# Optimization experiments

Measured on AMD Instinct MI355X. Metric: run time of the kernel, lower is better.

The kernel has to match this reference:

```python
import jax, jax.numpy as jnp
import numpy as np
from jax import lax

BITWIDTH = 7
EPS = 1e-5


def ti_quant(x):
    """TiFloatToInt8: per-tensor int8 quantization with power-of-2 scale."""
    rng = jnp.max(jnp.abs(x))
    bw = jnp.ceil(jnp.log2(rng))
    exp = bw - BITWIDTH
    q = jnp.clip(jnp.round(x * 2.0 ** (BITWIDTH - bw)), -128.0, 127.0)
    return q, exp


def ti_conv(xv, xe, wv, we, pad):
    """TiConv2d: integer conv (simulated in f32, all values int-valued),
    int32 accumulate, then shift back to 8 bits; exponents add."""
    acc = lax.conv_general_dilated(
        xv, wv, window_strides=(1, 1), padding=[(pad, pad), (pad, pad)],
        dimension_numbers=("NCHW", "OIHW", "NCHW"))
    rng = jnp.max(jnp.abs(acc))
    bw = jnp.ceil(jnp.log2(rng))
    shift = jnp.maximum(bw - BITWIDTH, 0.0)
    q = jnp.clip(jnp.round(acc * 2.0 ** (-shift)), -128.0, 127.0)
    return q, xe + we + shift


def batchnorm(x, gamma, beta):
    # training-mode BN: batch statistics over (N, H, W)
    mean = jnp.mean(x, axis=(0, 2, 3), keepdims=True)
    var = jnp.var(x, axis=(0, 2, 3), keepdims=True)
    g = gamma[None, :, None, None]
    b = beta[None, :, None, None]
    return g * (x - mean) * lax.rsqrt(var + EPS) + b


def setup_inputs() -> dict:
    key = jax.random.key(0)
    k0, k1, k2, k3, k4 = jax.random.split(key, 5)
    B, Cin, Cout, H, W = 32, 128, 256, 56, 56
    x_val = jax.random.randint(k0, (B, Cin, H, W), -128, 128, dtype=jnp.int32)
    x_exp = jnp.zeros((), jnp.float32) - 7.0
    wDW = jnp.round(jnp.clip(jax.random.normal(k1, (Cin, Cin, 3, 3), jnp.float32) * 32.0, -128.0, 127.0))
    wDW_exp = jnp.zeros((), jnp.float32) - 9.0
    wPW = jnp.round(jnp.clip(jax.random.normal(k2, (Cout, Cin, 1, 1), jnp.float32) * 32.0, -128.0, 127.0))
    wPW_exp = jnp.zeros((), jnp.float32) - 9.0
    gamma1 = jnp.ones((Cin,), jnp.float32) + 0.1 * jax.random.normal(k3, (Cin,), jnp.float32)
    beta1 = jnp.zeros((Cin,), jnp.float32)
    gamma2 = jnp.ones((Cout,), jnp.float32) + 0.1 * jax.random.normal(k4, (Cout,), jnp.float32)
    beta2 = jnp.zeros((Cout,), jnp.float32)
    return {"x_val": x_val, "x_exp": x_exp, "wDW": wDW, "wDW_exp": wDW_exp,
            "wPW": wPW, "wPW_exp": wPW_exp, "gamma1": gamma1, "beta1": beta1,
            "gamma2": gamma2, "beta2": beta2}


def reference(x_val, x_exp, wDW, wDW_exp, wPW, wPW_exp, gamma1, beta1, gamma2, beta2):
    xv = x_val.astype(jnp.float32)
    # convDW (3x3, in->in, pad=1)
    q, e = ti_conv(xv, x_exp, wDW, wDW_exp, 1)
    # dequant -> bn1 -> quant
    f = batchnorm(q * 2.0 ** e, gamma1, beta1)
    q, e = ti_quant(f)
    # TiReLU on int values
    q = jnp.maximum(q, 0.0)
    # convPW (1x1, in->out)
    q, e = ti_conv(q, e, wPW, wPW_exp, 0)
    # dequant -> bn2 -> quant -> relu
    f = batchnorm(q * 2.0 ** e, gamma2, beta2)
    q, e = ti_quant(f)
    q = jnp.maximum(q, 0.0)
    return q.astype(jnp.int8), e
```

## Files before the change

kernel.cpp:

```cpp
#include <hip/hip_runtime.h>
#include <cstdint>
#include <cstddef>

#define C1 128
#define C2 256
#define Hh 56
#define Wd 56
#define HW 3136
#define NHW 100352
#define N1 ((size_t)12845056)
#define N2 ((size_t)25690112)
#define XPSZ ((size_t)13778944)

typedef int v4i __attribute__((ext_vector_type(4)));
typedef int v16i __attribute__((ext_vector_type(16)));

static constexpr size_t OFF_XP = 0;
static constexpr size_t OFF_ACC1 = XPSZ;
static constexpr size_t OFF_Q1 = OFF_ACC1 + 4 * N1;
static constexpr size_t OFF_Q3 = OFF_Q1 + N1;
static constexpr size_t OFF_WQ1 = OFF_Q3 + N2;
static constexpr size_t OFF_WQ2 = OFF_WQ1 + 147456;
static constexpr size_t OFF_STATS = OFF_WQ2 + 32768;

struct Stats {
  int absmax1, absmax2, tick1, tick2;
  float scale1, e1, s2, e2;
  float scaleq2, e3, sf, ef;
  int sum1[C1]; unsigned sumsq1[C1];
  int min1[C1], max1[C1];
  float A1[C1], B1c[C1];
  int sum2[C2]; unsigned sumsq2[C2];
  int min2[C2], max2[C2];
  float A2[C2], B2c[C2];
};

__global__ __launch_bounds__(256) void k_pre(
    const int* __restrict__ x, signed char* __restrict__ xp,
    const float* __restrict__ wDW, signed char* __restrict__ wq1t,
    const float* __restrict__ wPW, signed char* __restrict__ wq2t,
    Stats* st) {
  __shared__ signed char lds[56 * 132];
  int t = threadIdx.x, bid = blockIdx.x;
  if (bid < 1856) {
    int hh = bid % 58, n = bid / 58;
    int* xpw = (int*)(xp + ((size_t)n * 58 + hh) * 7424);
    if (hh == 0 || hh == 57) {
      for (int o = t; o < 1856; o += 256) xpw[o] = 0;
      return;
    }
    int h = hh - 1;
    const int* xb = x + (size_t)n * C1 * HW + h * 56;
    for (int idx = t; idx < 7168; idx += 256) {
      int c = idx / 56, w = idx - c * 56;
      lds[w * 132 + c] = (signed char)xb[(size_t)c * HW + w];
    }
    __syncthreads();
    for (int o = t; o < 1856; o += 256) {
      int kb = o / 232, r = o - kb * 232, ww = r >> 2, cw = r & 3;
      int val = (ww == 0 || ww == 57) ? 0
                : *(const int*)&lds[(ww - 1) * 132 + kb * 16 + cw * 4];
      xpw[o] = val;
    }
    return;
  }
  if (bid < 2432) {
    int idx = (bid - 1856) * 256 + t;
    int co = idx / 1152, r = idx - co * 1152;
    int ci = r / 9, pos = r - ci * 9;
    int k = pos * 128 + ci;
    wq1t[(size_t)(k >> 4) * 2048 + co * 16 + (k & 15)] = (signed char)(int)wDW[idx];
    return;
  }
  if (bid < 2560) {
    int i = (bid - 2432) * 256 + t;
    int co = i >> 7, ci = i & 127;
    wq2t[(size_t)(ci >> 4) * 4096 + co * 16 + (ci & 15)] = (signed char)(int)wPW[i];
    return;
  }
  if (t == 0) { st->absmax1 = 0; st->absmax2 = 0; st->tick1 = 0; st->tick2 = 0; }
  for (int c = t; c < C1; c += 256) {
    st->sum1[c] = 0; st->sumsq1[c] = 0; st->min1[c] = 127; st->max1[c] = -128;
  }
  for (int c = t; c < C2; c += 256) {
    st->sum2[c] = 0; st->sumsq2[c] = 0; st->min2[c] = 127; st->max2[c] = -128;
  }
}

__device__ inline v4i ld16_lds(const signed char* p) {
  const int2* q = (const int2*)p;
  int2 lo = q[0], hi = q[1];
  v4i r; r[0] = lo.x; r[1] = lo.y; r[2] = hi.x; r[3] = hi.y;
  return r;
}

__device__ inline float bn_affine_v(int sum, unsigned sumsq, int mn, int mx,
                                    float g, float b, float e_in,
                                    float* Aout, float* Bout) {
  double meanq = (double)sum / (double)NHW;
  double varq = (double)sumsq / (double)NHW - meanq * meanq;
  float se = exp2f(e_in);
  float mean = (float)meanq * se;
  float var = (float)varq * se * se;
  float rsq = 1.0f / sqrtf(var + 1e-5f);
  float Avv = g * se * rsq;
  float Bvv = b - g * mean * rsq;
  *Aout = Avv; *Bout = Bvv;
  return fmaxf(fabsf(Avv * (float)mn + Bvv), fabsf(Avv * (float)mx + Bvv));
}

__global__ __launch_bounds__(256, 2) void k_conv1s(
    const signed char* __restrict__ xp, const signed char* __restrict__ wq1t,
    int* __restrict__ acc1, Stats* st) {
  __shared__ int reda[4];
  int t = threadIdx.x, lane = t & 63, wave = t >> 6;
  int half = lane >> 5, l31 = lane & 31;
  size_t g0 = (size_t)blockIdx.x * 256;

  const signed char* ab[2];
#pragma unroll
  for (int i = 0; i < 2; ++i) {
    size_t gm = g0 + wave * 64 + i * 32 + l31;
    int n = (int)(gm / HW);
    int p = (int)(gm - (size_t)n * HW);
    int h = p / 56, w = p - h * 56;
    ab[i] = xp + ((size_t)n * 58 + h) * 7424 + w * 16 + half * 928;
  }
  const signed char* bb[4];
#pragma unroll
  for (int j = 0; j < 4; ++j)
    bb[j] = wq1t + (size_t)(j * 32 + l31) * 16 + half * 2048;

  v16i a1[2][4];
#pragma unroll
  for (int i = 0; i < 2; ++i)
#pragma unroll
    for (int j = 0; j < 4; ++j)
#pragma unroll
      for (int r = 0; r < 16; ++r) a1[i][j][r] = 0;

#pragma unroll
  for (int pos = 0; pos < 9; ++pos) {
    int kh = pos / 3, kw = pos - kh * 3;
    const signed char* a0p = ab[0] + kh * 7424 + kw * 16;
    const signed char* a1p = ab[1] + kh * 7424 + kw * 16;
#pragma unroll
    for (int kb = 0; kb < 8; kb += 2) {
      v4i af0 = *(const v4i*)(a0p + kb * 928);
      v4i af1 = *(const v4i*)(a1p + kb * 928);
      v4i bf[4];
#pragma unroll
      for (int j = 0; j < 4; ++j)
        bf[j] = *(const v4i*)(bb[j] + pos * 16384 + kb * 2048);
#pragma unroll
      for (int j = 0; j < 4; ++j) {
        a1[0][j] = __builtin_amdgcn_mfma_i32_32x32x32_i8(af0, bf[j], a1[0][j], 0, 0, 0);
        a1[1][j] = __builtin_amdgcn_mfma_i32_32x32x32_i8(af1, bf[j], a1[1][j], 0, 0, 0);
      }
    }
  }

  int am = 0;
#pragma unroll
  for (int i = 0; i < 2; ++i)
#pragma unroll
    for (int j = 0; j < 4; ++j)
#pragma unroll
      for (int r = 0; r < 16; ++r) am = max(am, abs(a1[i][j][r]));
  for (int off = 32; off; off >>= 1) am = max(am, __shfl_down(am, off, 64));
  if (lane == 0) reda[wave] = am;
  __syncthreads();
  if (t == 0)
    atomicMax(&st->absmax1, max(max(reda[0], reda[1]), max(reda[2], reda[3])));

  int* ob = acc1 + (size_t)blockIdx.x * 32768;
#pragma unroll
  for (int i = 0; i < 2; ++i)
#pragma unroll
    for (int j = 0; j < 4; ++j)
#pragma unroll
      for (int reg = 0; reg < 16; ++reg)
        ob[(((wave * 2 + i) * 4 + j) * 16 + reg) * 64 + lane] = a1[i][j][reg];
}

__global__ __launch_bounds__(256, 2) void k_qstats1(
    const int* __restrict__ acc1, signed char* __restrict__ q1, Stats* st,
    const float* __restrict__ x_exp, const float* __restrict__ wDW_exp,
    const float* __restrict__ gamma1, const float* __restrict__ beta1) {
  __shared__ int qti[256 * 34];
  __shared__ int psum[C1], psq[C1], pmn[C1], pmx[C1];
  __shared__ float redc[2];
  __shared__ int lastf;
  signed char* qt = (signed char*)qti;
  int t = threadIdx.x, lane = t & 63, wave = t >> 6;
  int half = lane >> 5, l31 = lane & 31;

  if (t < C1) { psum[t] = 0; psq[t] = 0; pmn[t] = 127; pmx[t] = -128; }
  __syncthreads();

  int v1 = st->absmax1;
  int pw = 31 - __clz(v1 | 1);
  int bw = ((v1 & (v1 - 1)) == 0) ? pw : pw + 1;
  int sh = max(bw - 7, 0);
  float scale1 = exp2f((float)(-sh));
  float e1 = x_exp[0] + wDW_exp[0] + (float)sh;
  if (blockIdx.x == 0 && t == 0) st->e1 = e1;

  const int* ib = acc1 + (size_t)blockIdx.x * 32768;
#pragma unroll
  for (int j = 0; j < 4; ++j) {
    int sj = 0, sqj = 0, mnj = 127, mxj = -128;
    int c = j * 32 + l31;
#pragma unroll
    for (int i = 0; i < 2; ++i)
#pragma unroll
      for (int reg = 0; reg < 16; ++reg) {
        int av = ib[(((wave * 2 + i) * 4 + j) * 16 + reg) * 64 + lane];
        int row = (reg & 3) + 8 * (reg >> 2) + 4 * half;
        int pix = wave * 64 + i * 32 + row;
        float r = rintf((float)av * scale1);
        r = fminf(fmaxf(r, -128.f), 127.f);
        int qi = (int)r;
        qt[pix * 136 + c] = (signed char)qi;
        sj += qi; sqj += qi * qi; mnj = min(mnj, qi); mxj = max(mxj, qi);
      }
    sj += __shfl_down(sj, 32, 64);
    sqj += __shfl_down(sqj, 32, 64);
    mnj = min(mnj, __shfl_down(mnj, 32, 64));
    mxj = max(mxj, __shfl_down(mxj, 32, 64));
    if (half == 0) {
      atomicAdd(&psum[c], sj); atomicAdd(&psq[c], sqj);
      atomicMin(&pmn[c], mnj); atomicMax(&pmx[c], mxj);
    }
  }
  __syncthreads();
  if (t < C1) {
    atomicAdd(&st->sum1[t], psum[t]);
    atomicAdd(&st->sumsq1[t], (unsigned)psq[t]);
    atomicMin(&st->min1[t], pmn[t]);
    atomicMax(&st->max1[t], pmx[t]);
  }
  int* q1w = (int*)(q1 + (size_t)blockIdx.x * 256 * 128);
  for (int idx = t; idx < 8192; idx += 256)
    q1w[idx] = qti[(idx >> 5) * 34 + (idx & 31)];

  __syncthreads();
  if (t == 0) lastf = (atomicAdd(&st->tick1, 1) == 391);
  __syncthreads();
  if (lastf) {
    if (t < C1) {
      int sm = atomicAdd(&st->sum1[t], 0);
      unsigned sq = atomicAdd(&st->sumsq1[t], 0u);
      int mn = atomicMin(&st->min1[t], 127);
      int mx = atomicMax(&st->max1[t], -128);
      float cand = bn_affine_v(sm, sq, mn, mx, gamma1[t], beta1[t], e1,
                               &st->A1[t], &st->B1c[t]);
      for (int off = 32; off; off >>= 1) cand = fmaxf(cand, __shfl_down(cand, off, 64));
      if ((t & 63) == 0) redc[t >> 6] = cand;
    }
    __syncthreads();
    if (t == 0) {
      float rng = fmaxf(redc[0], redc[1]);
      float bwv = ceilf(log2f(rng));
      st->s2 = exp2f(7.0f - bwv);
      st->e2 = bwv - 7.0f;
    }
  }
}

template <int STORE>
__global__ __launch_bounds__(256, 2) void k_conv2t(
    const signed char* __restrict__ q1, const signed char* __restrict__ wq2t,
    signed char* __restrict__ q3, Stats* st, const float* __restrict__ wPW_exp,
    const float* __restrict__ gamma2, const float* __restrict__ beta2,
    float* __restrict__ out) {
  __shared__ int qti[128 * 34];
  __shared__ signed char stg[128 * 264];
  __shared__ int psum[C2], psq[C2], pmn[C2], pmx[C2];
  __shared__ int reda[4];
  __shared__ float red2[4];
  __shared__ int lastf;
  signed char* qt = (signed char*)qti;

  int t = threadIdx.x, lane = t & 63, wave = t >> 6;
  int half = lane >> 5, l31 = lane & 31;
  size_t g0 = (size_t)blockIdx.x * 128;

  if (STORE) { psum[t] = 0; psq[t] = 0; pmn[t] = 127; pmx[t] = -128; }

  int c4 = t & 31;
  float Av[4], Bv[4];
#pragma unroll
  for (int jj = 0; jj < 4; ++jj) {
    Av[jj] = st->A1[c4 * 4 + jj];
    Bv[jj] = st->B1c[c4 * 4 + jj];
  }
  float s2 = st->s2;
  const int* q1w = (const int*)(q1 + g0 * 128);
#pragma unroll
  for (int k = 0; k < 16; ++k) {
    int idx = k * 256 + t;
    int v = q1w[idx];
    int pix = idx >> 5;
    int outv = 0;
#pragma unroll
    for (int jj = 0; jj < 4; ++jj) {
      int b = (signed char)(v >> (8 * jj));
      float y = Av[jj] * (float)b + Bv[jj];
      float r = rintf(y * s2);
      r = fminf(fmaxf(r, -128.f), 127.f);
      r = fmaxf(r, 0.f);
      outv |= ((int)r & 0xff) << (8 * jj);
    }
    qti[pix * 34 + c4] = outv;
  }
  __syncthreads();

  v16i acc[8];
#pragma unroll
  for (int j = 0; j < 8; ++j)
#pragma unroll
    for (int r = 0; r < 16; ++r) acc[j][r] = 0;

#pragma unroll
  for (int ks = 0; ks < 4; ++ks) {
    v4i af = ld16_lds(&qt[(wave * 32 + l31) * 136 + half * 16 + ks * 32]);
#pragma unroll
    for (int j = 0; j < 8; ++j) {
      v4i bf = *(const v4i*)(wq2t + (size_t)(ks * 2 + half) * 4096 + (j * 32 + l31) * 16);
      acc[j] = __builtin_amdgcn_mfma_i32_32x32x32_i8(af, bf, acc[j], 0, 0, 0);
    }
  }

  if (STORE == 0) {
    int am2 = 0;
#pragma unroll
    for (int j = 0; j < 8; ++j)
#pragma unroll
      for (int r = 0; r < 16; ++r) am2 = max(am2, abs(acc[j][r]));
    for (int off = 32; off; off >>= 1) am2 = max(am2, __shfl_down(am2, off, 64));
    if (lane == 0) reda[wave] = am2;
    __syncthreads();
    if (t == 0)
      atomicMax(&st->absmax2, max(max(reda[0], reda[1]), max(reda[2], reda[3])));
  } else {
    int v2 = st->absmax2;
    int pw = 31 - __clz(v2 | 1);
    int bw = ((v2 & (v2 - 1)) == 0) ? pw : pw + 1;
    int sh2 = max(bw - 7, 0);
    float scale2 = exp2f((float)(-sh2));
    float e3 = st->e2 + wPW_exp[0] + (float)sh2;
    if (blockIdx.x == 0 && t == 0) st->e3 = e3;
#pragma unroll
    for (int j = 0; j < 8; ++j) {
      int c = j * 32 + l31;
      int sj = 0, sqj = 0, mnj = 127, mxj = -128;
#pragma unroll
      for (int reg = 0; reg < 16; ++reg) {
        int row = (reg & 3) + 8 * (reg >> 2) + 4 * half;
        float r = rintf((float)acc[j][reg] * scale2);
        r = fminf(fmaxf(r, -128.f), 127.f);
        int qi = (int)r;
        stg[(wave * 32 + row) * 264 + c] = (signed char)qi;
        sj += qi; sqj += qi * qi; mnj = min(mnj, qi); mxj = max(mxj, qi);
      }
      sj += __shfl_down(sj, 32, 64);
      sqj += __shfl_down(sqj, 32, 64);
      mnj = min(mnj, __shfl_down(mnj, 32, 64));
      mxj = max(mxj, __shfl_down(mxj, 32, 64));
      if (half == 0) {
        atomicAdd(&psum[c], sj); atomicAdd(&psq[c], sqj);
        atomicMin(&pmn[c], mnj); atomicMax(&pmx[c], mxj);
      }
    }
    __syncthreads();
    atomicAdd(&st->sum2[t], psum[t]);
    atomicAdd(&st->sumsq2[t], (unsigned)psq[t]);
    atomicMin(&st->min2[t], pmn[t]);
    atomicMax(&st->max2[t], pmx[t]);
    int* q3w = (int*)(q3 + g0 * 256);
#pragma unroll
    for (int k = 0; k < 32; ++k) {
      int idx = k * 256 + t;
      int pix = idx >> 6, cw = idx & 63;
      q3w[idx] = *(const int*)&stg[pix * 264 + cw * 4];
    }

    __syncthreads();
    if (t == 0) lastf = (atomicAdd(&st->tick2, 1) == 783);
    __syncthreads();
    if (lastf) {
      int sm = atomicAdd(&st->sum2[t], 0);
      unsigned sq = atomicAdd(&st->sumsq2[t], 0u);
      int mn = atomicMin(&st->min2[t], 127);
      int mx = atomicMax(&st->max2[t], -128);
      float cand = bn_affine_v(sm, sq, mn, mx, gamma2[t], beta2[t], e3,
                               &st->A2[t], &st->B2c[t]);
      for (int off = 32; off; off >>= 1) cand = fmaxf(cand, __shfl_down(cand, off, 64));
      if (lane == 0) red2[wave] = cand;
      __syncthreads();
      if (t == 0) {
        float rng = fmaxf(fmaxf(red2[0], red2[1]), fmaxf(red2[2], red2[3]));
        float bwv = ceilf(log2f(rng));
        st->sf = exp2f(7.0f - bwv);
        st->ef = bwv - 7.0f;
        out[N2] = bwv - 7.0f;
      }
    }
  }
}

__global__ __launch_bounds__(256) void k_out(
    const signed char* __restrict__ q3, const Stats* __restrict__ st,
    float* __restrict__ out) {
  __shared__ signed char lds[64 * 260];
  int t = threadIdx.x, lane = t & 63, wave = t >> 6;
  size_t g0 = (size_t)blockIdx.x * 64;
  int n = (int)(g0 / HW), p0 = (int)(g0 - (size_t)n * HW);
  const int* q3w = (const int*)(q3 + g0 * 256);
#pragma unroll
  for (int k = 0; k < 16; ++k) {
    int idx = k * 256 + t;
    int pix = idx >> 6, cw = idx & 63;
    *(int*)&lds[pix * 260 + cw * 4] = q3w[idx];
  }
  __syncthreads();
  float sf = st->sf;
  float* ob = out + (size_t)n * C2 * HW + p0 + lane;
#pragma unroll
  for (int cg = 0; cg < 16; ++cg) {
    int v = *(const int*)&lds[lane * 260 + wave * 64 + cg * 4];
#pragma unroll
    for (int jj = 0; jj < 4; ++jj) {
      int c = wave * 64 + cg * 4 + jj;
      float y = st->A2[c] * (float)((signed char)(v >> (8 * jj))) + st->B2c[c];
      float r = rintf(y * sf);
      r = fminf(fmaxf(r, -128.f), 127.f);
      ob[(size_t)c * HW] = fmaxf(r, 0.f);
    }
  }
}

extern "C" void kernel_launch(void* const* d_in, const int* in_sizes, int n_in,
                              void* d_out, int out_size, void* d_ws, size_t ws_size,
                              hipStream_t stream) {
  const int* x = (const int*)d_in[0];
  const float* x_exp = (const float*)d_in[1];
  const float* wDW = (const float*)d_in[2];
  const float* wDW_exp = (const float*)d_in[3];
  const float* wPW = (const float*)d_in[4];
  const float* wPW_exp = (const float*)d_in[5];
  const float* gamma1 = (const float*)d_in[6];
  const float* beta1 = (const float*)d_in[7];
  const float* gamma2 = (const float*)d_in[8];
  const float* beta2 = (const float*)d_in[9];
  float* out = (float*)d_out;

  char* ws = (char*)d_ws;
  signed char* xp2 = (signed char*)(ws + OFF_XP);
  int* acc1 = (int*)(ws + OFF_ACC1);
  signed char* q1 = (signed char*)(ws + OFF_Q1);
  signed char* q3 = (signed char*)(ws + OFF_Q3);
  signed char* wq1t = (signed char*)(ws + OFF_WQ1);
  signed char* wq2t = (signed char*)(ws + OFF_WQ2);
  Stats* st = (Stats*)(ws + OFF_STATS);

  hipLaunchKernelGGL(k_pre, dim3(2561), dim3(256), 0, stream,
                     x, xp2, wDW, wq1t, wPW, wq2t, st);
  hipLaunchKernelGGL(k_conv1s, dim3(392), dim3(256), 0, stream,
                     xp2, wq1t, acc1, st);
  hipLaunchKernelGGL(k_qstats1, dim3(392), dim3(256), 0, stream,
                     acc1, q1, st, x_exp, wDW_exp, gamma1, beta1);
  hipLaunchKernelGGL(HIP_KERNEL_NAME(k_conv2t<0>), dim3(784), dim3(256), 0, stream,
                     q1, wq2t, q3, st, wPW_exp, gamma2, beta2, out);
  hipLaunchKernelGGL(HIP_KERNEL_NAME(k_conv2t<1>), dim3(784), dim3(256), 0, stream,
                     q1, wq2t, q3, st, wPW_exp, gamma2, beta2, out);
  hipLaunchKernelGGL(k_out, dim3(1568), dim3(256), 0, stream, q3, st, out);
}
```

Before: 299.1 us.

## Halve per-block tiles in conv kernels to double grid and occupancy

Conv1 blocks now cover 128 pixels instead of 256, and qstats1 follows, so 784 blocks launch instead of 392. The pointwise conv is split by output-channel half into 1568 blocks, and the two template passes become separate kernels, conv2a and conv2b. Fewer accumulators per thread allow launch bounds of 4 blocks per CU, which should raise occupancy and fill the 256 CUs better. The cost is more redundant reloads of the activation tile and the q1 requantization, since both channel halves redo it, plus more global atomics.

```diff
diff --git a/kernel.cpp b/kernel.cpp
--- a/kernel.cpp
+++ b/kernel.cpp
@@ -109,85 +109,72 @@
   return fmaxf(fabsf(Avv * (float)mn + Bvv), fabsf(Avv * (float)mx + Bvv));
 }
 
-__global__ __launch_bounds__(256, 2) void k_conv1s(
+__global__ __launch_bounds__(256, 4) void k_conv1s(
     const signed char* __restrict__ xp, const signed char* __restrict__ wq1t,
     int* __restrict__ acc1, Stats* st) {
   __shared__ int reda[4];
   int t = threadIdx.x, lane = t & 63, wave = t >> 6;
   int half = lane >> 5, l31 = lane & 31;
-  size_t g0 = (size_t)blockIdx.x * 256;
-
-  const signed char* ab[2];
-#pragma unroll
-  for (int i = 0; i < 2; ++i) {
-    size_t gm = g0 + wave * 64 + i * 32 + l31;
-    int n = (int)(gm / HW);
-    int p = (int)(gm - (size_t)n * HW);
-    int h = p / 56, w = p - h * 56;
-    ab[i] = xp + ((size_t)n * 58 + h) * 7424 + w * 16 + half * 928;
-  }
+  size_t g0 = (size_t)blockIdx.x * 128;
+
+  size_t gm = g0 + wave * 32 + l31;
+  int n = (int)(gm / HW);
+  int p = (int)(gm - (size_t)n * HW);
+  int h = p / 56, w = p - h * 56;
+  const signed char* ap = xp + ((size_t)n * 58 + h) * 7424 + w * 16 + half * 928;
+
   const signed char* bb[4];
 #pragma unroll
   for (int j = 0; j < 4; ++j)
     bb[j] = wq1t + (size_t)(j * 32 + l31) * 16 + half * 2048;
 
-  v16i a1[2][4];
-#pragma unroll
-  for (int i = 0; i < 2; ++i)
-#pragma unroll
-    for (int j = 0; j < 4; ++j)
-#pragma unroll
-      for (int r = 0; r < 16; ++r) a1[i][j][r] = 0;
+  v16i a1[4];
+#pragma unroll
+  for (int j = 0; j < 4; ++j)
+#pragma unroll
+    for (int r = 0; r < 16; ++r) a1[j][r] = 0;
 
 #pragma unroll
   for (int pos = 0; pos < 9; ++pos) {
     int kh = pos / 3, kw = pos - kh * 3;
-    const signed char* a0p = ab[0] + kh * 7424 + kw * 16;
-    const signed char* a1p = ab[1] + kh * 7424 + kw * 16;
+    const signed char* a0p = ap + kh * 7424 + kw * 16;
 #pragma unroll
     for (int kb = 0; kb < 8; kb += 2) {
-      v4i af0 = *(const v4i*)(a0p + kb * 928);
-      v4i af1 = *(const v4i*)(a1p + kb * 928);
+      v4i af = *(const v4i*)(a0p + kb * 928);
       v4i bf[4];
 #pragma unroll
       for (int j = 0; j < 4; ++j)
         bf[j] = *(const v4i*)(bb[j] + pos * 16384 + kb * 2048);
 #pragma unroll
-      for (int j = 0; j < 4; ++j) {
-        a1[0][j] = __builtin_amdgcn_mfma_i32_32x32x32_i8(af0, bf[j], a1[0][j], 0, 0, 0);
-        a1[1][j] = __builtin_amdgcn_mfma_i32_32x32x32_i8(af1, bf[j], a1[1][j], 0, 0, 0);
-      }
+      for (int j = 0; j < 4; ++j)
+        a1[j] = __builtin_amdgcn_mfma_i32_32x32x32_i8(af, bf[j], a1[j], 0, 0, 0);
     }
   }
 
   int am = 0;
 #pragma unroll
-  for (int i = 0; i < 2; ++i)
-#pragma unroll
-    for (int j = 0; j < 4; ++j)
-#pragma unroll
-      for (int r = 0; r < 16; ++r) am = max(am, abs(a1[i][j][r]));
+  for (int j = 0; j < 4; ++j)
+#pragma unroll
+    for (int r = 0; r < 16; ++r) am = max(am, abs(a1[j][r]));
   for (int off = 32; off; off >>= 1) am = max(am, __shfl_down(am, off, 64));
   if (lane == 0) reda[wave] = am;
   __syncthreads();
   if (t == 0)
     atomicMax(&st->absmax1, max(max(reda[0], reda[1]), max(reda[2], reda[3])));
 
-  int* ob = acc1 + (size_t)blockIdx.x * 32768;
-#pragma unroll
-  for (int i = 0; i < 2; ++i)
-#pragma unroll
-    for (int j = 0; j < 4; ++j)
-#pragma unroll
-      for (int reg = 0; reg < 16; ++reg)
-        ob[(((wave * 2 + i) * 4 + j) * 16 + reg) * 64 + lane] = a1[i][j][reg];
-}
-
-__global__ __launch_bounds__(256, 2) void k_qstats1(
+  int* ob = acc1 + (size_t)blockIdx.x * 16384;
+#pragma unroll
+  for (int j = 0; j < 4; ++j)
+#pragma unroll
+    for (int reg = 0; reg < 16; ++reg)
+      ob[((wave * 4 + j) * 16 + reg) * 64 + lane] = a1[j][reg];
+}
+
+__global__ __launch_bounds__(256, 4) void k_qstats1(
     const int* __restrict__ acc1, signed char* __restrict__ q1, Stats* st,
     const float* __restrict__ x_exp, const float* __restrict__ wDW_exp,
     const float* __restrict__ gamma1, const float* __restrict__ beta1) {
-  __shared__ int qti[256 * 34];
+  __shared__ int qti[128 * 34];
   __shared__ int psum[C1], psq[C1], pmn[C1], pmx[C1];
   __shared__ float redc[2];
   __shared__ int lastf;
@@ -206,24 +193,22 @@
   float e1 = x_exp[0] + wDW_exp[0] + (float)sh;
   if (blockIdx.x == 0 && t == 0) st->e1 = e1;
 
-  const int* ib = acc1 + (size_t)blockIdx.x * 32768;
+  const int* ib = acc1 + (size_t)blockIdx.x * 16384;
 #pragma unroll
   for (int j = 0; j < 4; ++j) {
     int sj = 0, sqj = 0, mnj = 127, mxj = -128;
     int c = j * 32 + l31;
 #pragma unroll
-    for (int i = 0; i < 2; ++i)
-#pragma unroll
-      for (int reg = 0; reg < 16; ++reg) {
-        int av = ib[(((wave * 2 + i) * 4 + j) * 16 + reg) * 64 + lane];
-        int row = (reg & 3) + 8 * (reg >> 2) + 4 * half;
-        int pix = wave * 64 + i * 32 + row;
-        float r = rintf((float)av * scale1);
-        r = fminf(fmaxf(r, -128.f), 127.f);
-        int qi = (int)r;
-        qt[pix * 136 + c] = (signed char)qi;
-        sj += qi; sqj += qi * qi; mnj = min(mnj, qi); mxj = max(mxj, qi);
-      }
+    for (int reg = 0; reg < 16; ++reg) {
+      int av = ib[((wave * 4 + j) * 16 + reg) * 64 + lane];
+      int row = (reg & 3) + 8 * (reg >> 2) + 4 * half;
+      int pix = wave * 32 + row;
+      float r = rintf((float)av * scale1);
+      r = fminf(fmaxf(r, -128.f), 127.f);
+      int qi = (int)r;
+      qt[pix * 136 + c] = (signed char)qi;
+      sj += qi; sqj += qi * qi; mnj = min(mnj, qi); mxj = max(mxj, qi);
+    }
     sj += __shfl_down(sj, 32, 64);
     sqj += __shfl_down(sqj, 32, 64);
     mnj = min(mnj, __shfl_down(mnj, 32, 64));
@@ -240,12 +225,12 @@
     atomicMin(&st->min1[t], pmn[t]);
     atomicMax(&st->max1[t], pmx[t]);
   }
-  int* q1w = (int*)(q1 + (size_t)blockIdx.x * 256 * 128);
-  for (int idx = t; idx < 8192; idx += 256)
+  int* q1w = (int*)(q1 + (size_t)blockIdx.x * 16384);
+  for (int idx = t; idx < 4096; idx += 256)
     q1w[idx] = qti[(idx >> 5) * 34 + (idx & 31)];
 
   __syncthreads();
-  if (t == 0) lastf = (atomicAdd(&st->tick1, 1) == 391);
+  if (t == 0) lastf = (atomicAdd(&st->tick1, 1) == 783);
   __syncthreads();
   if (lastf) {
     if (t < C1) {
@@ -268,25 +253,16 @@
   }
 }
 
-template <int STORE>
-__global__ __launch_bounds__(256, 2) void k_conv2t(
+__global__ __launch_bounds__(256, 4) void k_conv2a(
     const signed char* __restrict__ q1, const signed char* __restrict__ wq2t,
-    signed char* __restrict__ q3, Stats* st, const float* __restrict__ wPW_exp,
-    const float* __restrict__ gamma2, const float* __restrict__ beta2,
-    float* __restrict__ out) {
+    Stats* st) {
   __shared__ int qti[128 * 34];
-  __shared__ signed char stg[128 * 264];
-  __shared__ int psum[C2], psq[C2], pmn[C2], pmx[C2];
   __shared__ int reda[4];
-  __shared__ float red2[4];
-  __shared__ int lastf;
   signed char* qt = (signed char*)qti;
-
   int t = threadIdx.x, lane = t & 63, wave = t >> 6;
   int half = lane >> 5, l31 = lane & 31;
-  size_t g0 = (size_t)blockIdx.x * 128;
-
-  if (STORE) { psum[t] = 0; psq[t] = 0; pmn[t] = 127; pmx[t] = -128; }
+  int gb = blockIdx.x >> 1, coh = blockIdx.x & 1;
+  size_t g0 = (size_t)gb * 128;
 
   int c4 = t & 31;
   float Av[4], Bv[4];
@@ -316,9 +292,9 @@
   }
   __syncthreads();
 
-  v16i acc[8];
-#pragma unroll
-  for (int j = 0; j < 8; ++j)
+  v16i acc[4];
+#pragma unroll
+  for (int j = 0; j < 4; ++j)
 #pragma unroll
     for (int r = 0; r < 16; ++r) acc[j][r] = 0;
 
@@ -326,86 +302,153 @@
   for (int ks = 0; ks < 4; ++ks) {
     v4i af = ld16_lds(&qt[(wave * 32 + l31) * 136 + half * 16 + ks * 32]);
 #pragma unroll
-    for (int j = 0; j < 8; ++j) {
-      v4i bf = *(const v4i*)(wq2t + (size_t)(ks * 2 + half) * 4096 + (j * 32 + l31) * 16);
+    for (int j = 0; j < 4; ++j) {
+      v4i bf = *(const v4i*)(wq2t + (size_t)(ks * 2 + half) * 4096 +
+                             (coh * 128 + j * 32 + l31) * 16);
       acc[j] = __builtin_amdgcn_mfma_i32_32x32x32_i8(af, bf, acc[j], 0, 0, 0);
     }
   }
 
-  if (STORE == 0) {
-    int am2 = 0;
-#pragma unroll
-    for (int j = 0; j < 8; ++j)
-#pragma unroll
-      for (int r = 0; r < 16; ++r) am2 = max(am2, abs(acc[j][r]));
-    for (int off = 32; off; off >>= 1) am2 = max(am2, __shfl_down(am2, off, 64));
-    if (lane == 0) reda[wave] = am2;
+  int am2 = 0;
+#pragma unroll
+  for (int j = 0; j < 4; ++j)
+#pragma unroll
+    for (int r = 0; r < 16; ++r) am2 = max(am2, abs(acc[j][r]));
+  for (int off = 32; off; off >>= 1) am2 = max(am2, __shfl_down(am2, off, 64));
+  if (lane == 0) reda[wave] = am2;
+  __syncthreads();
+  if (t == 0)
+    atomicMax(&st->absmax2, max(max(reda[0], reda[1]), max(reda[2], reda[3])));
+}
+
+__global__ __launch_bounds__(256, 4) void k_conv2b(
+    const signed char* __restrict__ q1, const signed char* __restrict__ wq2t,
+    signed char* __restrict__ q3, Stats* st, const float* __restrict__ wPW_exp,
+    const float* __restrict__ gamma2, const float* __restrict__ beta2,
+    float* __restrict__ out) {
+  __shared__ int qti[128 * 34];
+  __shared__ __align__(16) signed char stg[128 * 132];
+  __shared__ int psum[C1], psq[C1], pmn[C1], pmx[C1];
+  __shared__ float red2[4];
+  __shared__ int lastf;
+  signed char* qt = (signed char*)qti;
+
+  int t = threadIdx.x, lane = t & 63, wave = t >> 6;
+  int half = lane >> 5, l31 = lane & 31;
+  int gb = blockIdx.x >> 1, coh = blockIdx.x & 1;
+  size_t g0 = (size_t)gb * 128;
+
+  if (t < C1) { psum[t] = 0; psq[t] = 0; pmn[t] = 127; pmx[t] = -128; }
+
+  int c4 = t & 31;
+  float Av[4], Bv[4];
+#pragma unroll
+  for (int jj = 0; jj < 4; ++jj) {
+    Av[jj] = st->A1[c4 * 4 + jj];
+    Bv[jj] = st->B1c[c4 * 4 + jj];
+  }
+  float s2 = st->s2;
+  const int* q1w = (const int*)(q1 + g0 * 128);
+#pragma unroll
+  for (int k = 0; k < 16; ++k) {
+    int idx = k * 256 + t;
+    int v = q1w[idx];
+    int pix = idx >> 5;
+    int outv = 0;
+#pragma unroll
+    for (int jj = 0; jj < 4; ++jj) {
+      int b = (signed char)(v >> (8 * jj));
+      float y = Av[jj] * (float)b + Bv[jj];
+      float r = rintf(y * s2);
+      r = fminf(fmaxf(r, -128.f), 127.f);
+      r = fmaxf(r, 0.f);
+      outv |= ((int)r & 0xff) << (8 * jj);
+    }
+    qti[pix * 34 + c4] = outv;
+  }
+  __syncthreads();
+
+  v16i acc[4];
+#pragma unroll
+  for (int j = 0; j < 4; ++j)
+#pragma unroll
+    for (int r = 0; r < 16; ++r) acc[j][r] = 0;
+
+#pragma unroll
+  for (int ks = 0; ks < 4; ++ks) {
+    v4i af = ld16_lds(&qt[(wave * 32 + l31) * 136 + half * 16 + ks * 32]);
+#pragma unroll
+    for (int j = 0; j < 4; ++j) {
+      v4i bf = *(const v4i*)(wq2t + (size_t)(ks * 2 + half) * 4096 +
+                             (coh * 128 + j * 32 + l31) * 16);
+      acc[j] = __builtin_amdgcn_mfma_i32_32x32x32_i8(af, bf, acc[j], 0, 0, 0);
+    }
+  }
+
+  int v2 = st->absmax2;
+  int pw = 31 - __clz(v2 | 1);
+  int bw = ((v2 & (v2 - 1)) == 0) ? pw : pw + 1;
+  int sh2 = max(bw - 7, 0);
+  float scale2 = exp2f((float)(-sh2));
+  float e3 = st->e2 + wPW_exp[0] + (float)sh2;
+  if (blockIdx.x == 0 && t == 0) st->e3 = e3;
+
+#pragma unroll
+  for (int j = 0; j < 4; ++j) {
+    int cl = j * 32 + l31;
+    int sj = 0, sqj = 0, mnj = 127, mxj = -128;
+#pragma unroll
+    for (int reg = 0; reg < 16; ++reg) {
+      int row = (reg & 3) + 8 * (reg >> 2) + 4 * half;
+      float r = rintf((float)acc[j][reg] * scale2);
+      r = fminf(fmaxf(r, -128.f), 127.f);
+      int qi = (int)r;
+      stg[(wave * 32 + row) * 132 + cl] = (signed char)qi;
+      sj += qi; sqj += qi * qi; mnj = min(mnj, qi); mxj = max(mxj, qi);
+    }
+    sj += __shfl_down(sj, 32, 64);
+    sqj += __shfl_down(sqj, 32, 64);
+    mnj = min(mnj, __shfl_down(mnj, 32, 64));
+    mxj = max(mxj, __shfl_down(mxj, 32, 64));
+    if (half == 0) {
+      atomicAdd(&psum[cl], sj); atomicAdd(&psq[cl], sqj);
+      atomicMin(&pmn[cl], mnj); atomicMax(&pmx[cl], mxj);
+    }
+  }
+  __syncthreads();
+  if (t < C1) {
+    atomicAdd(&st->sum2[coh * 128 + t], psum[t]);
+    atomicAdd(&st->sumsq2[coh * 128 + t], (unsigned)psq[t]);
+    atomicMin(&st->min2[coh * 128 + t], pmn[t]);
+    atomicMax(&st->max2[coh * 128 + t], pmx[t]);
+  }
+  int* q3w = (int*)(q3 + g0 * 256);
+#pragma unroll
+  for (int k = 0; k < 16; ++k) {
+    int idx = k * 256 + t;
+    int pix = idx >> 5, cw = idx & 31;
+    q3w[pix * 64 + coh * 32 + cw] = *(const int*)&stg[pix * 132 + cw * 4];
+  }
+
+  __syncthreads();
+  if (t == 0) lastf = (atomicAdd(&st->tick2, 1) == 1567);
+  __syncthreads();
+  if (lastf) {
+    int sm = atomicAdd(&st->sum2[t], 0);
+    unsigned sq = atomicAdd(&st->sumsq2[t], 0u);
+    int mn = atomicMin(&st->min2[t], 127);
+    int mx = atomicMax(&st->max2[t], -128);
+    float cand = bn_affine_v(sm, sq, mn, mx, gamma2[t], beta2[t], e3,
+                             &st->A2[t], &st->B2c[t]);
+    for (int off = 32; off; off >>= 1) cand = fmaxf(cand, __shfl_down(cand, off, 64));
+    if (lane == 0) red2[wave] = cand;
     __syncthreads();
-    if (t == 0)
-      atomicMax(&st->absmax2, max(max(reda[0], reda[1]), max(reda[2], reda[3])));
-  } else {
-    int v2 = st->absmax2;
-    int pw = 31 - __clz(v2 | 1);
-    int bw = ((v2 & (v2 - 1)) == 0) ? pw : pw + 1;
-    int sh2 = max(bw - 7, 0);
-    float scale2 = exp2f((float)(-sh2));
-    float e3 = st->e2 + wPW_exp[0] + (float)sh2;
-    if (blockIdx.x == 0 && t == 0) st->e3 = e3;
-#pragma unroll
-    for (int j = 0; j < 8; ++j) {
-      int c = j * 32 + l31;
-      int sj = 0, sqj = 0, mnj = 127, mxj = -128;
-#pragma unroll
-      for (int reg = 0; reg < 16; ++reg) {
-        int row = (reg & 3) + 8 * (reg >> 2) + 4 * half;
-        float r = rintf((float)acc[j][reg] * scale2);
-        r = fminf(fmaxf(r, -128.f), 127.f);
-        int qi = (int)r;
-        stg[(wave * 32 + row) * 264 + c] = (signed char)qi;
-        sj += qi; sqj += qi * qi; mnj = min(mnj, qi); mxj = max(mxj, qi);
-      }
-      sj += __shfl_down(sj, 32, 64);
-      sqj += __shfl_down(sqj, 32, 64);
-      mnj = min(mnj, __shfl_down(mnj, 32, 64));
-      mxj = max(mxj, __shfl_down(mxj, 32, 64));
-      if (half == 0) {
-        atomicAdd(&psum[c], sj); atomicAdd(&psq[c], sqj);
-        atomicMin(&pmn[c], mnj); atomicMax(&pmx[c], mxj);
-      }
-    }
-    __syncthreads();
-    atomicAdd(&st->sum2[t], psum[t]);
-    atomicAdd(&st->sumsq2[t], (unsigned)psq[t]);
-    atomicMin(&st->min2[t], pmn[t]);
-    atomicMax(&st->max2[t], pmx[t]);
-    int* q3w = (int*)(q3 + g0 * 256);
-#pragma unroll
-    for (int k = 0; k < 32; ++k) {
-      int idx = k * 256 + t;
-      int pix = idx >> 6, cw = idx & 63;
-      q3w[idx] = *(const int*)&stg[pix * 264 + cw * 4];
-    }
-
-    __syncthreads();
-    if (t == 0) lastf = (atomicAdd(&st->tick2, 1) == 783);
-    __syncthreads();
-    if (lastf) {
-      int sm = atomicAdd(&st->sum2[t], 0);
-      unsigned sq = atomicAdd(&st->sumsq2[t], 0u);
-      int mn = atomicMin(&st->min2[t], 127);
-      int mx = atomicMax(&st->max2[t], -128);
-      float cand = bn_affine_v(sm, sq, mn, mx, gamma2[t], beta2[t], e3,
-                               &st->A2[t], &st->B2c[t]);
-      for (int off = 32; off; off >>= 1) cand = fmaxf(cand, __shfl_down(cand, off, 64));
-      if (lane == 0) red2[wave] = cand;
-      __syncthreads();
-      if (t == 0) {
-        float rng = fmaxf(fmaxf(red2[0], red2[1]), fmaxf(red2[2], red2[3]));
-        float bwv = ceilf(log2f(rng));
-        st->sf = exp2f(7.0f - bwv);
-        st->ef = bwv - 7.0f;
-        out[N2] = bwv - 7.0f;
-      }
+    if (t == 0) {
+      float rng = fmaxf(fmaxf(red2[0], red2[1]), fmaxf(red2[2], red2[3]));
+      float bwv = ceilf(log2f(rng));
+      st->sf = exp2f(7.0f - bwv);
+      st->ef = bwv - 7.0f;
+      out[N2] = bwv - 7.0f;
     }
   }
 }
@@ -467,13 +510,13 @@
 
   hipLaunchKernelGGL(k_pre, dim3(2561), dim3(256), 0, stream,
                      x, xp2, wDW, wq1t, wPW, wq2t, st);
-  hipLaunchKernelGGL(k_conv1s, dim3(392), dim3(256), 0, stream,
+  hipLaunchKernelGGL(k_conv1s, dim3(784), dim3(256), 0, stream,
                      xp2, wq1t, acc1, st);
-  hipLaunchKernelGGL(k_qstats1, dim3(392), dim3(256), 0, stream,
+  hipLaunchKernelGGL(k_qstats1, dim3(784), dim3(256), 0, stream,
                      acc1, q1, st, x_exp, wDW_exp, gamma1, beta1);
-  hipLaunchKernelGGL(HIP_KERNEL_NAME(k_conv2t<0>), dim3(784), dim3(256), 0, stream,
-                     q1, wq2t, q3, st, wPW_exp, gamma2, beta2, out);
-  hipLaunchKernelGGL(HIP_KERNEL_NAME(k_conv2t<1>), dim3(784), dim3(256), 0, stream,
+  hipLaunchKernelGGL(k_conv2a, dim3(1568), dim3(256), 0, stream,
+                     q1, wq2t, st);
+  hipLaunchKernelGGL(k_conv2b, dim3(1568), dim3(256), 0, stream,
                      q1, wq2t, q3, st, wPW_exp, gamma2, beta2, out);
   hipLaunchKernelGGL(k_out, dim3(1568), dim3(256), 0, stream, q3, st, out);
 }
```

Measured after the change: 306.7 us. 2.5% more time.
